# Performance work log

Measured on AMD Instinct MI355X. Metric: run time of the kernel, lower is better.

## Reference

```python
import jax, jax.numpy as jnp
import numpy as np

B, N, D_IN, D_HID, N_ITER = 32, 512, 256, 128, 10


def setup_inputs() -> dict:
    key = jax.random.key(0)
    ks = jax.random.split(key, 8)
    s = 1.0 / np.sqrt(D_IN)  # torch Linear default init range
    return {
        "Xh": jax.random.normal(ks[0], (B, N, D_IN), jnp.float32),
        "Xm": jax.random.normal(ks[1], (B, N, D_IN), jnp.float32),
        # position 0 is the root; tokens 1..len are valid
        "lengths": jax.random.randint(ks[2], (B,), N // 2, N),
        "Wh": jax.random.uniform(ks[3], (D_HID, D_IN), jnp.float32, -s, s),
        "bh": jax.random.uniform(ks[4], (D_HID,), jnp.float32, -s, s),
        "Wm": jax.random.uniform(ks[5], (D_HID, D_IN), jnp.float32, -s, s),
        "bm": jax.random.uniform(ks[6], (D_HID,), jnp.float32, -s, s),
        "V": 0.01 * jax.random.normal(ks[7], (D_HID, D_HID), jnp.float32),
    }


def _logZ(scores, lengths):
    """Matrix-tree log-partition for single-root nonprojective trees.

    scores: [B,N,N] arc scores, scores[b,h,m] = head h -> modifier m, index 0 = root.
    lengths: [B] number of real tokens (valid modifiers at 1..len).
    """
    Bn, Nn, _ = scores.shape
    idx = jnp.arange(Nn)
    tok = (idx[None, :] >= 1) & (idx[None, :] <= lengths[:, None])   # [B,N] valid modifiers
    head = idx[None, :] <= lengths[:, None]                          # [B,N] valid heads (incl. root)
    pair = head[:, :, None] & tok[:, None, :] & (idx[:, None] != idx[None, :])
    # stability shift: every tree has exactly `len` edges, so logZ shifts by len*c
    c = jax.lax.stop_gradient(
        jnp.max(jnp.where(pair, scores, -jnp.inf), axis=(1, 2)))
    A = jnp.where(pair, jnp.exp(scores - c[:, None, None]), 0.0)     # [B,N,N]
    r = A[:, 0, 1:]                                                  # root -> token weights [B,N-1]
    At = A[:, 1:, 1:]                                                # token -> token weights
    ar = jnp.arange(Nn - 1)
    # Laplacian L = diag(colsum) - At (diag of At is zero by pair mask)
    Lap = (-At).at[:, ar, ar].set(r + At.sum(axis=1))
    # Koo et al. (2007): replace first row with root weights
    Lhat = Lap.at[:, 0, :].set(r)
    # padded positions: identity rows to keep det unchanged
    Lhat = Lhat.at[:, ar, ar].add(jnp.where(tok[:, 1:], 0.0, 1.0))
    _, logabs = jnp.linalg.slogdet(Lhat)
    return logabs + lengths.astype(scores.dtype) * c


def _marginals(scores, lengths):
    """nonprojective_marginals: (logZ, entropy, mu) via grad of logZ."""
    def f(s):
        lz = _logZ(s, lengths)
        return lz.sum(), lz
    (_, logZ), Y = jax.value_and_grad(f, has_aux=True)(scores)
    entr = logZ - jnp.sum(Y * scores, axis=(1, 2))
    return logZ, entr, Y


def reference(Xh, Xm, lengths, Wh, bh, Wm, bm, V):
    # dropout=0 -> H_mask/M_mask are ones
    H0 = Xh @ Wh.T + bh          # h_mlp(Xh), invariant across iterations
    M0 = Xm @ Wm.T + bm          # m_mlp(Xm)
    H = jax.nn.relu(H0)
    M = jax.nn.relu(M0)
    scores = jnp.einsum("bhu,uv,bmv->bhm", H, V, M)
    logZ, entr, Y = _marginals(scores, lengths)
    for _ in range(1, N_ITER):
        Hn = jax.nn.relu(H0 + Y @ M @ V.T)                       # _update_H
        Mn = jax.nn.relu(M0 + jnp.swapaxes(Y, -2, -1) @ H @ V)   # _update_M
        scores = jnp.einsum("bhu,uv,bmv->bhm", Hn, V, Mn)
        logZ, entr, Y = _marginals(scores, lengths)
        H, M = Hn, Mn
    return scores, logZ, Y, entr
```

## Files before the change

### kernel.cpp

```cpp
#include <hip/hip_runtime.h>
#include <math.h>

constexpr int BB = 32;
constexpr int NN_ = 512;
constexpr int DIN = 256;
constexpr int DH = 128;
constexpr int NITER = 10;
constexpr long HSTR = (long)NN_ * DH;
constexpr long SSTR = (long)NN_ * NN_;
constexpr long LSTR = 512L * 512L;

__device__ __forceinline__ unsigned f2mono(float f) {
    unsigned u = __float_as_uint(f);
    return (u & 0x80000000u) ? ~u : (u | 0x80000000u);
}
__device__ __forceinline__ float mono2f(unsigned u) {
    return __uint_as_float((u & 0x80000000u) ? (u & 0x7fffffffu) : ~u);
}

__device__ __forceinline__ float invert128(float r[8][8], int tid,
        float (*RowP)[8][132], float (*ColPT)[8][132], float (*Rnew)[8][132])
{
    int tx = tid & 15, ty = tid >> 4;
    int lane = tid & 63, w = tid >> 6;
    int li = lane >> 3, lj = lane & 7;
    const bool act = (tid < 256);
    float lacc = 0.f;
    __syncthreads();
    for (int s8 = 0; s8 < 16; ++s8) {
        int p = s8 & 1;
        if (act && ty == s8) {
            #pragma unroll
            for (int i = 0; i < 8; ++i)
                #pragma unroll
                for (int j = 0; j < 8; ++j)
                    RowP[p][i][tx * 8 + j] = r[i][j];
        }
        if (act && tx == s8) {
            float sub = (ty == s8) ? 1.f : 0.f;
            #pragma unroll
            for (int i = 0; i < 8; ++i)
                #pragma unroll
                for (int j = 0; j < 8; ++j)
                    ColPT[p][j][ty * 8 + i] = r[i][j] - ((i == j) ? sub : 0.f);
        }
        __syncthreads();
        float d = RowP[p][li][s8 * 8 + lj];
        float prod = 1.f;
        #pragma unroll
        for (int s = 0; s < 8; ++s) {
            float pv = __shfl(d, s * 9);
            prod *= pv;
            float pinv = 1.0f / pv;
            float rv = __shfl(d, s * 8 + lj);
            float cv = __shfl(d, li * 8 + s);
            float nd;
            if (li == s && lj == s)  nd = pinv;
            else if (li == s)        nd = rv * pinv;
            else if (lj == s)        nd = -cv * pinv;
            else                     nd = d - cv * pinv * rv;
            d = nd;
        }
        lacc += logf(fabsf(prod));
        if (act) {
            int sr = li;
            int jq = w * 32 + lj * 4;
            float dsr[8];
            #pragma unroll
            for (int t = 0; t < 8; ++t) dsr[t] = __shfl(d, (lane & 56) + t);
            float a0 = 0.f, a1 = 0.f, a2 = 0.f, a3 = 0.f;
            #pragma unroll
            for (int t = 0; t < 8; ++t) {
                float4 rp = *(const float4*)&RowP[p][t][jq];
                a0 += dsr[t] * rp.x; a1 += dsr[t] * rp.y;
                a2 += dsr[t] * rp.z; a3 += dsr[t] * rp.w;
            }
            if ((jq >> 3) == s8) {
                if ((jq & 7) == 0) {
                    a0 = dsr[0] + ((sr == 0) ? 1.f : 0.f);
                    a1 = dsr[1] + ((sr == 1) ? 1.f : 0.f);
                    a2 = dsr[2] + ((sr == 2) ? 1.f : 0.f);
                    a3 = dsr[3] + ((sr == 3) ? 1.f : 0.f);
                } else {
                    a0 = dsr[4] + ((sr == 4) ? 1.f : 0.f);
                    a1 = dsr[5] + ((sr == 5) ? 1.f : 0.f);
                    a2 = dsr[6] + ((sr == 6) ? 1.f : 0.f);
                    a3 = dsr[7] + ((sr == 7) ? 1.f : 0.f);
                }
            }
            *(float4*)&Rnew[p][sr][jq] = make_float4(a0, a1, a2, a3);
        }
        __syncthreads();
        if (act) {
            #pragma unroll
            for (int t = 0; t < 8; ++t) {
                float cp[8], rn[8];
                *(float4*)&cp[0] = *(const float4*)&ColPT[p][t][ty * 8];
                *(float4*)&cp[4] = *(const float4*)&ColPT[p][t][ty * 8 + 4];
                *(float4*)&rn[0] = *(const float4*)&Rnew[p][t][tx * 8];
                *(float4*)&rn[4] = *(const float4*)&Rnew[p][t][tx * 8 + 4];
                #pragma unroll
                for (int i = 0; i < 8; ++i)
                    #pragma unroll
                    for (int j = 0; j < 8; ++j)
                        r[i][j] -= cp[i] * rn[j];
            }
        }
    }
    return lacc;
}

template<int AMODE, int BMODE, int EPI>
__global__ __launch_bounds__(256) void gemm64(
    const float* __restrict__ A, const float* __restrict__ Bm,
    float* __restrict__ C, const float* __restrict__ Dp, float* __restrict__ C2,
    int Mdim, int Ndim, int Kdim,
    long sA, long sB, long sC, long sD)
{
    constexpr int BK = 16;
    __shared__ float As[BK][64 + 4];
    __shared__ float Bs[BK][64 + 4];
    int b = blockIdx.z;
    const float* Ab = A + (long)b * sA;
    const float* Bb = Bm + (long)b * sB;
    int m0 = blockIdx.x * 64, n0 = blockIdx.y * 64;
    int tid = threadIdx.x;
    int tx = tid & 15, ty = tid >> 4;
    float acc[4][4] = {};

    int arow, acol, brow, bcol;
    if (AMODE == 0) { arow = tid >> 2; acol = (tid & 3) * 4; }
    else            { arow = tid >> 4; acol = (tid & 15) * 4; }
    if (BMODE == 0) { brow = tid >> 4; bcol = (tid & 15) * 4; }
    else            { brow = tid >> 2; bcol = (tid & 3) * 4; }

    float4 av, bv;
    if (AMODE == 0) av = *(const float4*)(Ab + (long)(m0 + arow) * Kdim + acol);
    else            av = *(const float4*)(Ab + (long)(0 + arow) * Mdim + m0 + acol);
    if (BMODE == 0) bv = *(const float4*)(Bb + (long)(0 + brow) * Ndim + n0 + bcol);
    else            bv = *(const float4*)(Bb + (long)(n0 + brow) * Kdim + bcol);

    for (int k0 = 0; k0 < Kdim; k0 += BK) {
        __syncthreads();
        if (AMODE == 0) {
            As[acol + 0][arow] = av.x; As[acol + 1][arow] = av.y;
            As[acol + 2][arow] = av.z; As[acol + 3][arow] = av.w;
        } else {
            *(float4*)&As[arow][acol] = av;
        }
        if (BMODE == 0) {
            *(float4*)&Bs[brow][bcol] = bv;
        } else {
            Bs[bcol + 0][brow] = bv.x; Bs[bcol + 1][brow] = bv.y;
            Bs[bcol + 2][brow] = bv.z; Bs[bcol + 3][brow] = bv.w;
        }
        float4 av2, bv2;
        if (k0 + BK < Kdim) {
            int k1 = k0 + BK;
            if (AMODE == 0) av2 = *(const float4*)(Ab + (long)(m0 + arow) * Kdim + k1 + acol);
            else            av2 = *(const float4*)(Ab + (long)(k1 + arow) * Mdim + m0 + acol);
            if (BMODE == 0) bv2 = *(const float4*)(Bb + (long)(k1 + brow) * Ndim + n0 + bcol);
            else            bv2 = *(const float4*)(Bb + (long)(n0 + brow) * Kdim + k1 + bcol);
        }
        __syncthreads();
        #pragma unroll
        for (int k = 0; k < BK; ++k) {
            float4 a4 = *(const float4*)&As[k][ty * 4];
            float4 b4 = *(const float4*)&Bs[k][tx * 4];
            float avv[4] = {a4.x, a4.y, a4.z, a4.w};
            float bvv[4] = {b4.x, b4.y, b4.z, b4.w};
            #pragma unroll
            for (int i = 0; i < 4; ++i)
                #pragma unroll
                for (int j = 0; j < 4; ++j)
                    acc[i][j] += avv[i] * bvv[j];
        }
        av = av2; bv = bv2;
    }

    int r0 = m0 + ty * 4, c0 = n0 + tx * 4;
    if (EPI == 0) {
        float* Cb = C + (long)b * sC;
        #pragma unroll
        for (int i = 0; i < 4; ++i)
            *(float4*)(Cb + (long)(r0 + i) * Ndim + c0) =
                make_float4(acc[i][0], acc[i][1], acc[i][2], acc[i][3]);
    } else if (EPI == 1) {
        float4 bias = *(const float4*)(Dp + c0);
        float bb4[4] = {bias.x, bias.y, bias.z, bias.w};
        #pragma unroll
        for (int i = 0; i < 4; ++i) {
            float pre[4];
            #pragma unroll
            for (int j = 0; j < 4; ++j) pre[j] = acc[i][j] + bb4[j];
            *(float4*)(C2 + (long)(r0 + i) * Ndim + c0) =
                make_float4(pre[0], pre[1], pre[2], pre[3]);
            *(float4*)(C + (long)(r0 + i) * Ndim + c0) =
                make_float4(fmaxf(pre[0], 0.f), fmaxf(pre[1], 0.f),
                            fmaxf(pre[2], 0.f), fmaxf(pre[3], 0.f));
        }
    } else {
        const float* Db = Dp + (long)b * sD;
        float* Cb = C + (long)b * sC;
        #pragma unroll
        for (int i = 0; i < 4; ++i) {
            float4 d = *(const float4*)(Db + (long)(r0 + i) * Ndim + c0);
            float pre[4] = {acc[i][0] + d.x, acc[i][1] + d.y,
                            acc[i][2] + d.z, acc[i][3] + d.w};
            *(float4*)(Cb + (long)(r0 + i) * Ndim + c0) =
                make_float4(fmaxf(pre[0], 0.f), fmaxf(pre[1], 0.f),
                            fmaxf(pre[2], 0.f), fmaxf(pre[3], 0.f));
        }
    }
}

template<int AMODE>
__global__ __launch_bounds__(256) void gemm32(
    const float* __restrict__ A, const float* __restrict__ Bm,
    float* __restrict__ C, const float* __restrict__ Dp,
    int Mdim, int Ndim, int Kdim,
    long sA, long sB, long sC, long sD)
{
    constexpr int BK = 16;
    __shared__ float As[BK][36];
    __shared__ float Bs[BK][68];
    int b = blockIdx.z;
    const float* Ab = A + (long)b * sA;
    const float* Bb = Bm + (long)b * sB;
    int m0 = blockIdx.x * 32, n0 = blockIdx.y * 64;
    int tid = threadIdx.x;
    int tx = tid & 15, ty = tid >> 4;
    float acc[2][4] = {};

    int arow, acol;
    if (AMODE == 0) { arow = tid >> 2; acol = (tid & 3) * 4; }
    else            { arow = tid >> 3; acol = (tid & 7) * 4; }
    bool aload = (tid < 128);
    int brow = tid >> 4, bcol = (tid & 15) * 4;

    float4 av, bv;
    if (aload) {
        if (AMODE == 0) av = *(const float4*)(Ab + (long)(m0 + arow) * Kdim + acol);
        else            av = *(const float4*)(Ab + (long)arow * Mdim + m0 + acol);
    }
    bv = *(const float4*)(Bb + (long)brow * Ndim + n0 + bcol);

    for (int k0 = 0; k0 < Kdim; k0 += BK) {
        __syncthreads();
        if (aload) {
            if (AMODE == 0) {
                As[acol + 0][arow] = av.x; As[acol + 1][arow] = av.y;
                As[acol + 2][arow] = av.z; As[acol + 3][arow] = av.w;
            } else {
                *(float4*)&As[arow][acol] = av;
            }
        }
        *(float4*)&Bs[brow][bcol] = bv;
        float4 av2, bv2;
        if (k0 + BK < Kdim) {
            int k1 = k0 + BK;
            if (aload) {
                if (AMODE == 0) av2 = *(const float4*)(Ab + (long)(m0 + arow) * Kdim + k1 + acol);
                else            av2 = *(const float4*)(Ab + (long)(k1 + arow) * Mdim + m0 + acol);
            }
            bv2 = *(const float4*)(Bb + (long)(k1 + brow) * Ndim + n0 + bcol);
        }
        __syncthreads();
        #pragma unroll
        for (int k = 0; k < BK; ++k) {
            float a0 = As[k][ty * 2], a1 = As[k][ty * 2 + 1];
            float4 b4 = *(const float4*)&Bs[k][tx * 4];
            float bb[4] = {b4.x, b4.y, b4.z, b4.w};
            #pragma unroll
            for (int j = 0; j < 4; ++j) {
                acc[0][j] += a0 * bb[j];
                acc[1][j] += a1 * bb[j];
            }
        }
        av = av2; bv = bv2;
    }

    int r0 = m0 + ty * 2, c0 = n0 + tx * 4;
    const float* Db = Dp + (long)b * sD;
    float* Cb = C + (long)b * sC;
    #pragma unroll
    for (int i = 0; i < 2; ++i) {
        float4 d = *(const float4*)(Db + (long)(r0 + i) * Ndim + c0);
        float pre[4] = {acc[i][0] + d.x, acc[i][1] + d.y,
                        acc[i][2] + d.z, acc[i][3] + d.w};
        *(float4*)(Cb + (long)(r0 + i) * Ndim + c0) =
            make_float4(fmaxf(pre[0], 0.f), fmaxf(pre[1], 0.f),
                        fmaxf(pre[2], 0.f), fmaxf(pre[3], 0.f));
    }
}

__global__ __launch_bounds__(256) void score_gemm(
    const float* __restrict__ A, const float* __restrict__ Bm,
    float* __restrict__ C, const int* __restrict__ len,
    unsigned* __restrict__ cu)
{
    int b = blockIdx.z;
    const float* Ab = A + (long)b * HSTR;
    const float* Bb = Bm + (long)b * HSTR;
    int m0 = blockIdx.x * 128, n0 = blockIdx.y * 128;
    int tid = threadIdx.x, tx = tid & 15, ty = tid >> 4;
    __shared__ float As[8][132];
    __shared__ float Bs[8][132];
    float acc[8][8] = {};
    int row = tid >> 1, kq = (tid & 1) << 2;
    float4 av = *(const float4*)(Ab + (long)(m0 + row) * DH + kq);
    float4 bv = *(const float4*)(Bb + (long)(n0 + row) * DH + kq);
    for (int kc = 0; kc < DH; kc += 8) {
        __syncthreads();
        As[kq + 0][row] = av.x; As[kq + 1][row] = av.y;
        As[kq + 2][row] = av.z; As[kq + 3][row] = av.w;
        Bs[kq + 0][row] = bv.x; Bs[kq + 1][row] = bv.y;
        Bs[kq + 2][row] = bv.z; Bs[kq + 3][row] = bv.w;
        float4 av2, bv2;
        if (kc + 8 < DH) {
            av2 = *(const float4*)(Ab + (long)(m0 + row) * DH + kc + 8 + kq);
            bv2 = *(const float4*)(Bb + (long)(n0 + row) * DH + kc + 8 + kq);
        }
        __syncthreads();
        #pragma unroll
        for (int k = 0; k < 8; ++k) {
            float a[8], bb[8];
            *(float4*)&a[0] = *(float4*)&As[k][ty * 8];
            *(float4*)&a[4] = *(float4*)&As[k][ty * 8 + 4];
            *(float4*)&bb[0] = *(float4*)&Bs[k][tx * 8];
            *(float4*)&bb[4] = *(float4*)&Bs[k][tx * 8 + 4];
            #pragma unroll
            for (int i = 0; i < 8; ++i)
                #pragma unroll
                for (int j = 0; j < 8; ++j) acc[i][j] += a[i] * bb[j];
        }
        av = av2; bv = bv2;
    }
    int L = len[b];
    float vmax = -3.0e38f;
    float* Cb = C + (long)b * SSTR;
    #pragma unroll
    for (int i = 0; i < 8; ++i) {
        int h = m0 + ty * 8 + i;
        bool hok = (h <= L);
        *(float4*)(Cb + (long)h * NN_ + n0 + tx * 8) =
            make_float4(acc[i][0], acc[i][1], acc[i][2], acc[i][3]);
        *(float4*)(Cb + (long)h * NN_ + n0 + tx * 8 + 4) =
            make_float4(acc[i][4], acc[i][5], acc[i][6], acc[i][7]);
        #pragma unroll
        for (int j = 0; j < 8; ++j) {
            int m = n0 + tx * 8 + j;
            if (hok && m >= 1 && m <= L && m != h) vmax = fmaxf(vmax, acc[i][j]);
        }
    }
    __syncthreads();
    float* red = &As[0][0];
    red[tid] = vmax; __syncthreads();
    for (int off = 128; off; off >>= 1) {
        if (tid < off) red[tid] = fmaxf(red[tid], red[tid + off]);
        __syncthreads();
    }
    if (tid == 0) atomicMax(&cu[b], f2mono(red[0]));
}

__global__ void zero_scal(float* scal) {
    if (threadIdx.x < 96) scal[threadIdx.x] = 0.f;
}

__global__ __launch_bounds__(256) void colsum_k(const float* __restrict__ sc,
                                                const int* __restrict__ len,
                                                const unsigned* __restrict__ cu,
                                                float* __restrict__ colsum)
{
    int b = blockIdx.x, yb = blockIdx.y;
    int tid = threadIdx.x, lane = tid & 63, w = tid >> 6;
    int L = len[b];
    float c = mono2f(cu[b]);
    int m = yb * 64 + lane;
    const float* S = sc + (long)b * SSTR;
    float s = 0.f;
    bool mv = (m >= 1 && m <= L);
    if (mv) {
        for (int h = 1 + w; h < NN_; h += 4) {
            if (h <= L && h != m) s += expf(S[(long)h * NN_ + m] - c);
        }
    }
    __shared__ float part[4][64];
    part[w][lane] = s; __syncthreads();
    if (tid < 64)
        colsum[(long)b * NN_ + yb * 64 + tid] =
            part[0][tid] + part[1][tid] + part[2][tid] + part[3][tid];
}

__global__ __launch_bounds__(256) void build_diag0(const float* __restrict__ sc,
                                                   const int* __restrict__ len,
                                                   const unsigned* __restrict__ cu,
                                                   const float* __restrict__ colsum,
                                                   float* __restrict__ Lm,
                                                   float* __restrict__ logdet)
{
    __shared__ float sm[6][8][132];
    int b = blockIdx.x;
    int tid = threadIdx.x;
    int L = len[b];
    float c = mono2f(cu[b]);
    const float* S = sc + (long)b * SSTR;
    const float* cs = colsum + (long)b * NN_;
    int tx = tid & 15, ty = tid >> 4;
    float r[8][8];
    #pragma unroll
    for (int i = 0; i < 8; ++i) {
        int gi = ty * 8 + i;
        #pragma unroll
        for (int j = 0; j < 8; ++j) {
            int gj = tx * 8 + j;
            int tm = gj + 1;
            bool mv = (tm <= L);
            float v;
            if (gi == 0) {
                v = mv ? expf(S[tm] - c) : 0.f;
            } else if (gi == gj) {
                float rv = mv ? expf(S[tm] - c) : 0.f;
                v = rv + cs[tm] + (mv ? 0.f : 1.f);
            } else {
                int h = gi + 1;
                v = (h <= L && mv) ? -expf(S[(long)h * NN_ + tm] - c) : 0.f;
            }
            r[i][j] = v;
        }
    }
    float lacc = invert128(r, tid,
                           (float(*)[8][132])&sm[0],
                           (float(*)[8][132])&sm[2],
                           (float(*)[8][132])&sm[4]);
    float* Ab = Lm + (long)b * LSTR;
    #pragma unroll
    for (int i = 0; i < 8; ++i) {
        *(float4*)(Ab + (long)(ty * 8 + i) * 512 + tx * 8) =
            make_float4(r[i][0], r[i][1], r[i][2], r[i][3]);
        *(float4*)(Ab + (long)(ty * 8 + i) * 512 + tx * 8 + 4) =
            make_float4(r[i][4], r[i][5], r[i][6], r[i][7]);
    }
    if (tid == 0) atomicAdd(&logdet[b], lacc);
}

__global__ __launch_bounds__(256) void build_rows(const float* __restrict__ sc,
                                                  const int* __restrict__ len,
                                                  const unsigned* __restrict__ cu,
                                                  const float* __restrict__ colsum,
                                                  float* __restrict__ Lm,
                                                  float* __restrict__ Fb0)
{
    int b = blockIdx.x;
    int tid = threadIdx.x;
    int L = len[b];
    float c = mono2f(cu[b]);
    const float* S = sc + (long)b * SSTR;
    const float* cs = colsum + (long)b * NN_;

    int i0 = blockIdx.y * 8;
    #pragma unroll
    for (int r = 0; r < 8; ++r) {
        int i = i0 + r;
        float* Lrow = Lm + (long)b * LSTR + (long)i * 512;
        float* Frow = Fb0 + (long)b * HSTR + (long)i * 128;
        #pragma unroll
        for (int q = 0; q < 2; ++q) {
            int j = tid + q * 256;
            float v;
            if (i == 511 || j == 511) {
                v = (i == j) ? 1.f : 0.f;
            } else {
                int tm = j + 1;
                bool mv = (tm <= L);
                if (i == 0) {
                    v = mv ? expf(S[tm] - c) : 0.f;
                } else if (i == j) {
                    float rv = mv ? expf(S[tm] - c) : 0.f;
                    v = rv + cs[tm] + ((tm > L) ? 1.f : 0.f);
                } else {
                    int h = i + 1;
                    v = (h <= L && mv) ? -expf(S[(long)h * NN_ + tm] - c) : 0.f;
                }
            }
            if (!(i < 128 && j < 128)) Lrow[j] = v;
            if (q == 0 && j < 128 && i >= 128) Frow[j] = v;
        }
    }
}

__global__ __launch_bounds__(256) void gj_panel(float* __restrict__ Lm,
                                                float* __restrict__ Fnext, int kb)
{
    constexpr int BK = 16;
    __shared__ float Ds[BK][132];
    __shared__ float As2[BK][36];
    int b = blockIdx.x;
    int j = blockIdx.y >> 2;
    int cq = blockIdx.y & 3;
    int jt = j + (j >= kb);
    int c0 = cq * 32;
    int tid = threadIdx.x;
    int tx = tid & 7, ty = tid >> 3;
    float* base = Lm + (long)b * LSTR;
    const float* D = base + (long)(kb * 128) * 512 + kb * 128;
    float* Aj = base + (long)(kb * 128) * 512 + jt * 128;
    int drow = tid >> 1, dk8 = (tid & 1) * 8;
    int akr = tid >> 3, acq4 = (tid & 7) * 4;
    bool aload = (akr < BK);
    float acc[4][4] = {};
    float4 dva = *(const float4*)(D + (long)drow * 512 + dk8);
    float4 dvb = *(const float4*)(D + (long)drow * 512 + dk8 + 4);
    float4 av;
    if (aload) av = *(const float4*)(Aj + (long)akr * 512 + c0 + acq4);
    for (int kc = 0; kc < 128; kc += BK) {
        __syncthreads();
        Ds[dk8 + 0][drow] = dva.x; Ds[dk8 + 1][drow] = dva.y;
        Ds[dk8 + 2][drow] = dva.z; Ds[dk8 + 3][drow] = dva.w;
        Ds[dk8 + 4][drow] = dvb.x; Ds[dk8 + 5][drow] = dvb.y;
        Ds[dk8 + 6][drow] = dvb.z; Ds[dk8 + 7][drow] = dvb.w;
        if (aload) *(float4*)&As2[akr][acq4] = av;
        float4 dva2, dvb2, av2;
        if (kc + BK < 128) {
            dva2 = *(const float4*)(D + (long)drow * 512 + kc + BK + dk8);
            dvb2 = *(const float4*)(D + (long)drow * 512 + kc + BK + dk8 + 4);
            if (aload) av2 = *(const float4*)(Aj + (long)(kc + BK + akr) * 512 + c0 + acq4);
        }
        __syncthreads();
        #pragma unroll
        for (int k = 0; k < BK; ++k) {
            float4 a4 = *(const float4*)&Ds[k][ty * 4];
            float4 b4 = *(const float4*)&As2[k][tx * 4];
            float a[4] = {a4.x, a4.y, a4.z, a4.w};
            float bb[4] = {b4.x, b4.y, b4.z, b4.w};
            #pragma unroll
            for (int i = 0; i < 4; ++i)
                #pragma unroll
                for (int jj = 0; jj < 4; ++jj)
                    acc[i][jj] += a[i] * bb[jj];
        }
        dva = dva2; dvb = dvb2; av = av2;
    }
    bool dual = (jt == kb + 1);
    float* Fn = Fnext + (long)b * HSTR + (long)(kb * 128) * 128;
    #pragma unroll
    for (int i = 0; i < 4; ++i) {
        float4 o = make_float4(acc[i][0], acc[i][1], acc[i][2], acc[i][3]);
        *(float4*)(Aj + (long)(ty * 4 + i) * 512 + c0 + tx * 4) = o;
        if (dual) *(float4*)(Fn + (long)(ty * 4 + i) * 128 + c0 + tx * 4) = o;
    }
}

__global__ __launch_bounds__(256) void gj_update64(
    float* __restrict__ Lm, const float* __restrict__ Fbuf,
    float* __restrict__ Fnext, float* __restrict__ logdet, int kb)
{
    constexpr int BK = 16;
    __shared__ float sm[6 * 8 * 132];
    int b = blockIdx.x;
    int tid = threadIdx.x;
    float* base = Lm + (long)b * LSTR;

    if (blockIdx.z == 0) {
        if (blockIdx.y != 0 || kb >= 3) return;
        int dt = kb + 1;
        const float* F = Fbuf + (long)b * HSTR + (long)(dt * 128) * 128;
        const float* R = base + (long)(kb * 128) * 512 + dt * 128;
        float* Cb = base + (long)(dt * 128) * 512 + dt * 128;
        float (*Fs)[132] = (float (*)[132])sm;
        float (*Rs)[132] = (float (*)[132])(sm + 16 * 132);
        int tx = tid & 15, ty = tid >> 4;
        int frow = tid >> 1, fkq = (tid & 1) << 3;
        int rkr = tid >> 4, rcq = (tid & 15) << 3;
        float acc[8][8] = {};
        float4 fva = *(const float4*)(F + (long)frow * 128 + fkq);
        float4 fvb = *(const float4*)(F + (long)frow * 128 + fkq + 4);
        float4 rva = *(const float4*)(R + (long)rkr * 512 + rcq);
        float4 rvb = *(const float4*)(R + (long)rkr * 512 + rcq + 4);
        for (int kc = 0; kc < 128; kc += BK) {
            __syncthreads();
            Fs[fkq + 0][frow] = fva.x; Fs[fkq + 1][frow] = fva.y;
            Fs[fkq + 2][frow] = fva.z; Fs[fkq + 3][frow] = fva.w;
            Fs[fkq + 4][frow] = fvb.x; Fs[fkq + 5][frow] = fvb.y;
            Fs[fkq + 6][frow] = fvb.z; Fs[fkq + 7][frow] = fvb.w;
            *(float4*)&Rs[rkr][rcq] = rva;
            *(float4*)&Rs[rkr][rcq + 4] = rvb;
            float4 fva2, fvb2, rva2, rvb2;
            if (kc + BK < 128) {
                fva2 = *(const float4*)(F + (long)frow * 128 + kc + BK + fkq);
                fvb2 = *(const float4*)(F + (long)frow * 128 + kc + BK + fkq + 4);
                rva2 = *(const float4*)(R + (long)(kc + BK + rkr) * 512 + rcq);
                rvb2 = *(const float4*)(R + (long)(kc + BK + rkr) * 512 + rcq + 4);
            }
            __syncthreads();
            #pragma unroll
            for (int k = 0; k < BK; ++k) {
                float a[8], bb[8];
                *(float4*)&a[0] = *(const float4*)&Fs[k][ty * 8];
                *(float4*)&a[4] = *(const float4*)&Fs[k][ty * 8 + 4];
                *(float4*)&bb[0] = *(const float4*)&Rs[k][tx * 8];
                *(float4*)&bb[4] = *(const float4*)&Rs[k][tx * 8 + 4];
                #pragma unroll
                for (int i = 0; i < 8; ++i)
                    #pragma unroll
                    for (int j = 0; j < 8; ++j)
                        acc[i][j] += a[i] * bb[j];
            }
            fva = fva2; fvb = fvb2; rva = rva2; rvb = rvb2;
        }
        #pragma unroll
        for (int i = 0; i < 8; ++i) {
            float4 o0 = *(const float4*)(Cb + (long)(ty * 8 + i) * 512 + tx * 8);
            float4 o1 = *(const float4*)(Cb + (long)(ty * 8 + i) * 512 + tx * 8 + 4);
            acc[i][0] = o0.x - acc[i][0]; acc[i][1] = o0.y - acc[i][1];
            acc[i][2] = o0.z - acc[i][2]; acc[i][3] = o0.w - acc[i][3];
            acc[i][4] = o1.x - acc[i][4]; acc[i][5] = o1.y - acc[i][5];
            acc[i][6] = o1.z - acc[i][6]; acc[i][7] = o1.w - acc[i][7];
        }
        float lacc = invert128(acc, tid,
                               (float (*)[8][132])sm,
                               (float (*)[8][132])(sm + 2 * 8 * 132),
                               (float (*)[8][132])(sm + 4 * 8 * 132));
        #pragma unroll
        for (int i = 0; i < 8; ++i) {
            *(float4*)(Cb + (long)(ty * 8 + i) * 512 + tx * 8) =
                make_float4(acc[i][0], acc[i][1], acc[i][2], acc[i][3]);
            *(float4*)(Cb + (long)(ty * 8 + i) * 512 + tx * 8 + 4) =
                make_float4(acc[i][4], acc[i][5], acc[i][6], acc[i][7]);
        }
        if (tid == 0) atomicAdd(&logdet[b], lacc);
        return;
    }

    float (*Fs)[68] = (float (*)[68])sm;
    float (*Rs)[68] = (float (*)[68])(sm + BK * 68);
    int it = blockIdx.y;
    int ib = it + (it >= kb);
    int sub = blockIdx.z - 1;
    int jt = sub >> 2;
    int quad = sub & 3;
    if (kb < 3 && ib == kb + 1 && jt == kb + 1) return;
    int r0 = (quad >> 1) * 64, c0 = (quad & 1) * 64;
    int tx = tid & 15, ty = tid >> 4;
    const float* F = Fbuf + (long)b * HSTR + (long)(ib * 128 + r0) * 128;
    const float* R = base + (long)(kb * 128) * 512 + jt * 128 + c0;
    float* Cb = base + (long)(ib * 128 + r0) * 512 + jt * 128 + c0;
    int frow = tid >> 2, fkq = (tid & 3) << 2;
    int rkr = tid >> 4, rcq = (tid & 15) << 2;
    float acc[4][4] = {};
    float4 fv = *(const float4*)(F + (long)frow * 128 + fkq);
    float4 rv = *(const float4*)(R + (long)rkr * 512 + rcq);
    for (int kc = 0; kc < 128; kc += BK) {
        __syncthreads();
        Fs[fkq + 0][frow] = fv.x; Fs[fkq + 1][frow] = fv.y;
        Fs[fkq + 2][frow] = fv.z; Fs[fkq + 3][frow] = fv.w;
        *(float4*)&Rs[rkr][rcq] = rv;
        float4 fv2, rv2;
        if (kc + BK < 128) {
            fv2 = *(const float4*)(F + (long)frow * 128 + kc + BK + fkq);
            rv2 = *(const float4*)(R + (long)(kc + BK + rkr) * 512 + rcq);
        }
        __syncthreads();
        #pragma unroll
        for (int k = 0; k < BK; ++k) {
            float4 a4 = *(const float4*)&Fs[k][ty * 4];
            float4 b4 = *(const float4*)&Rs[k][tx * 4];
            float a[4] = {a4.x, a4.y, a4.z, a4.w};
            float bb[4] = {b4.x, b4.y, b4.z, b4.w};
            #pragma unroll
            for (int i = 0; i < 4; ++i)
                #pragma unroll
                for (int j = 0; j < 4; ++j)
                    acc[i][j] += a[i] * bb[j];
        }
        fv = fv2; rv = rv2;
    }
    bool dual = (jt == kb + 1);
    float* Fn = Fnext + (long)b * HSTR + (long)(ib * 128 + r0) * 128 + c0;
    if (jt == kb) {
        #pragma unroll
        for (int i = 0; i < 4; ++i)
            *(float4*)(Cb + (long)(ty * 4 + i) * 512 + tx * 4) =
                make_float4(-acc[i][0], -acc[i][1], -acc[i][2], -acc[i][3]);
    } else {
        #pragma unroll
        for (int i = 0; i < 4; ++i) {
            float4 o = *(const float4*)(Cb + (long)(ty * 4 + i) * 512 + tx * 4);
            o = make_float4(o.x - acc[i][0], o.y - acc[i][1],
                            o.z - acc[i][2], o.w - acc[i][3]);
            *(float4*)(Cb + (long)(ty * 4 + i) * 512 + tx * 4) = o;
            if (dual) *(float4*)(Fn + (long)(ty * 4 + i) * 128 + tx * 4) = o;
        }
    }
}

__global__ __launch_bounds__(256) void y_k(const float* __restrict__ sc,
                                           const float* __restrict__ Binv,
                                           const int* __restrict__ len,
                                           const unsigned* __restrict__ cu,
                                           float* __restrict__ Y,
                                           float* __restrict__ Ssum)
{
    int b = blockIdx.x;
    int ht = blockIdx.y >> 3, mt = blockIdx.y & 7;
    int h0 = ht * 64, m0 = mt * 64;
    int tid = threadIdx.x;
    int L = len[b];
    float c = mono2f(cu[b]);
    const float* S = sc + (long)b * SSTR;
    const float* Bi = Binv + (long)b * LSTR;
    float* Yb = Y + (long)b * SSTR;
    __shared__ float Bs[64][65];
    __shared__ float Ds[64], C0s[64];
    {
        int hh = tid & 63, m4 = tid >> 6;
        int col = h0 + hh - 1;
        for (int mm = m4; mm < 64; mm += 4) {
            int row = m0 + mm - 1;
            Bs[mm][hh] = (row >= 0 && col >= 0) ? Bi[(long)row * 512 + col] : 0.f;
        }
    }
    if (tid < 64) {
        int row = m0 + tid - 1;
        Ds[tid] = (row >= 0) ? Bi[(long)row * 512 + row] : 0.f;
    } else if (tid < 128) {
        int mm = tid - 64, row = m0 + mm - 1;
        C0s[mm] = (row >= 0) ? Bi[(long)row * 512] : 0.f;
    }
    __syncthreads();
    int mm = tid & 63, hq = tid >> 6;
    int m = m0 + mm;
    float lsum = 0.f;
    bool mvalid = (m >= 1 && m <= L);
    float dterm = (m >= 2) ? Ds[mm] : 0.f;
    #pragma unroll
    for (int hi = 0; hi < 16; ++hi) {
        int hh = hq * 16 + hi;
        int h = h0 + hh;
        float s = S[(long)h * NN_ + m];
        float y = 0.f;
        if (mvalid && h <= L && h != m) {
            float a = expf(s - c);
            float g;
            if (h == 0) g = C0s[mm] + dterm;
            else g = dterm - ((h >= 2) ? Bs[mm][hh] : 0.f);
            y = a * g;
        }
        Yb[(long)h * NN_ + m] = y;
        lsum += y * s;
    }
    __shared__ float red[256];
    red[tid] = lsum; __syncthreads();
    for (int off = 128; off; off >>= 1) {
        if (tid < off) red[tid] += red[tid + off];
        __syncthreads();
    }
    if (tid == 0) atomicAdd(&Ssum[b], red[0]);
}

__global__ void fin_k(const int* __restrict__ len, unsigned* __restrict__ cu,
                      float* __restrict__ logdet, float* __restrict__ Ssum,
                      float* __restrict__ outLogZ, float* __restrict__ outEntr)
{
    int b = threadIdx.x;
    if (b < 32) {
        float c = mono2f(cu[b]);
        float lz = logdet[b] + (float)len[b] * c;
        outLogZ[b] = lz;
        outEntr[b] = lz - Ssum[b];
        cu[b] = 0u;
        logdet[b] = 0.f;
        Ssum[b] = 0.f;
    }
}

extern "C" void kernel_launch(void* const* d_in, const int* in_sizes, int n_in,
                              void* d_out, int out_size, void* d_ws, size_t ws_size,
                              hipStream_t stream)
{
    const float* Xh = (const float*)d_in[0];
    const float* Xm = (const float*)d_in[1];
    const int*   len = (const int*)d_in[2];
    const float* Wh = (const float*)d_in[3];
    const float* bh = (const float*)d_in[4];
    const float* Wm = (const float*)d_in[5];
    const float* bm = (const float*)d_in[6];
    const float* V  = (const float*)d_in[7];

    float* ws = (float*)d_ws;
    constexpr long U = 2097152;
    float* H0 = ws;
    float* M0 = ws + U;
    float* Ha = ws + 2 * U;
    float* Ma = ws + 3 * U;
    float* Hb = ws + 4 * U;
    float* Mb = ws + 5 * U;
    float* T1 = ws + 6 * U;
    float* Yt = ws + 7 * U;
    float* Lm = ws + 8 * U;
    float* cs = ws + 12 * U;
    float* scal = ws + 12 * U + 16384;
    unsigned* cu = (unsigned*)scal;
    float* logdet = scal + 32;
    float* Ssum = scal + 64;

    float* Sout = (float*)d_out;
    float* outLogZ = (float*)d_out + 8388608;
    float* Yout = (float*)d_out + 8388640;
    float* outEntr = (float*)d_out + 8388640 + 8388608;

    zero_scal<<<1, 96, 0, stream>>>(scal);

    gemm64<0,1,1><<<dim3(256, 2, 1), 256, 0, stream>>>(
        Xh, Wh, Ha, bh, H0, 16384, DH, DIN, 0, 0, 0, 0);
    gemm64<0,1,1><<<dim3(256, 2, 1), 256, 0, stream>>>(
        Xm, Wm, Ma, bm, M0, 16384, DH, DIN, 0, 0, 0, 0);

    float* Hc = Ha; float* Mc = Ma; float* Hn = Hb; float* Mn = Mb;
    for (int t = 0; t < NITER; ++t) {
        if (t > 0) {
            gemm64<0,1,0><<<dim3(8,2,BB),256,0,stream>>>(
                Mc, V, Yt, nullptr, nullptr, 512, DH, DH, HSTR, 0, HSTR, 0);
            gemm32<0><<<dim3(16,2,BB),256,0,stream>>>(
                Yout, Yt, Hn, H0, 512, DH, 512, SSTR, HSTR, HSTR, HSTR);
            gemm32<1><<<dim3(16,2,BB),256,0,stream>>>(
                Yout, T1, Mn, M0, 512, DH, 512, SSTR, HSTR, HSTR, HSTR);
            { float* tmp = Hc; Hc = Hn; Hn = tmp; }
            { float* tmp = Mc; Mc = Mn; Mn = tmp; }
        }
        gemm64<0,0,0><<<dim3(8,2,BB),256,0,stream>>>(
            Hc, V, T1, nullptr, nullptr, 512, DH, DH, HSTR, 0, HSTR, 0);
        score_gemm<<<dim3(4,4,BB),256,0,stream>>>(T1, Mc, Sout, len, cu);

        colsum_k<<<dim3(BB,8),256,0,stream>>>(Sout, len, cu, cs);
        build_diag0<<<dim3(BB),256,0,stream>>>(Sout, len, cu, cs, Lm, logdet);
        build_rows<<<dim3(BB,64),256,0,stream>>>(Sout, len, cu, cs, Lm, Yt);

        float* Fbufs[2] = {Yt, Hn};
        for (int kb = 0; kb < 4; ++kb) {
            float* Fcur  = Fbufs[kb & 1];
            float* Fnext = Fbufs[(kb + 1) & 1];
            gj_panel<<<dim3(BB,12),256,0,stream>>>(Lm, Fnext, kb);
            gj_update64<<<dim3(BB,3,17),256,0,stream>>>(Lm, Fcur, Fnext, logdet, kb);
        }
        y_k<<<dim3(BB,64),256,0,stream>>>(Sout, Lm, len, cu, Yout, Ssum);
        fin_k<<<1,32,0,stream>>>(len, cu, logdet, Ssum, outLogZ, outEntr);
    }
}
```

Before: 5.538 ms.

## Move next diagonal-block inversion into panel kernel to shorten critical path

The lookahead step (updating and inverting the next 128x128 diagonal block) moves from the update kernel into an extra block of the panel kernel. That block computes D·A for the next column panel into scratch, then applies the Schur update and inversion. The update kernel can then start without a long-running inversion block trailing behind it. The cost is recomputing the panel product redundantly in one block, and it adds a scratch buffer (reusing Mn) plus a threadfence. The dual-write panel tile now goes only to Fnext, and the update kernel reads it from there.

```diff
diff --git a/kernel.cpp b/kernel.cpp
--- a/kernel.cpp
+++ b/kernel.cpp
@@ -489,20 +489,146 @@
     }
 }
 
-__global__ __launch_bounds__(256) void gj_panel(float* __restrict__ Lm,
-                                                float* __restrict__ Fnext, int kb)
+__global__ __launch_bounds__(256) void gj_panel(
+    float* __restrict__ Lm, const float* __restrict__ Fcur,
+    float* __restrict__ Fnext, float* __restrict__ Rscr,
+    float* __restrict__ logdet, int kb)
 {
     constexpr int BK = 16;
-    __shared__ float Ds[BK][132];
-    __shared__ float As2[BK][36];
+    __shared__ float sm[6 * 8 * 132];
     int b = blockIdx.x;
+    int tid = threadIdx.x;
+    float* base = Lm + (long)b * LSTR;
+
+    if (blockIdx.y == 12) {
+        if (kb >= 3) return;
+        int dt = kb + 1;
+        int tx = tid & 15, ty = tid >> 4;
+        float (*Xs)[132] = (float (*)[132])sm;
+        float (*Ys)[132] = (float (*)[132])(sm + 16 * 132);
+        int xr = tid >> 1, xk = (tid & 1) << 3;
+        int yk = tid >> 4, yc = (tid & 15) << 3;
+        float* Rb = Rscr + (long)b * 16384;
+        {
+            const float* Dv = base + (long)(kb * 128) * 512 + kb * 128;
+            const float* Am = base + (long)(kb * 128) * 512 + dt * 128;
+            float acc[8][8] = {};
+            float4 xa = *(const float4*)(Dv + (long)xr * 512 + xk);
+            float4 xb = *(const float4*)(Dv + (long)xr * 512 + xk + 4);
+            float4 ya = *(const float4*)(Am + (long)yk * 512 + yc);
+            float4 yb = *(const float4*)(Am + (long)yk * 512 + yc + 4);
+            for (int kc = 0; kc < 128; kc += BK) {
+                __syncthreads();
+                Xs[xk + 0][xr] = xa.x; Xs[xk + 1][xr] = xa.y;
+                Xs[xk + 2][xr] = xa.z; Xs[xk + 3][xr] = xa.w;
+                Xs[xk + 4][xr] = xb.x; Xs[xk + 5][xr] = xb.y;
+                Xs[xk + 6][xr] = xb.z; Xs[xk + 7][xr] = xb.w;
+                *(float4*)&Ys[yk][yc] = ya;
+                *(float4*)&Ys[yk][yc + 4] = yb;
+                float4 xa2, xb2, ya2, yb2;
+                if (kc + BK < 128) {
+                    xa2 = *(const float4*)(Dv + (long)xr * 512 + kc + BK + xk);
+                    xb2 = *(const float4*)(Dv + (long)xr * 512 + kc + BK + xk + 4);
+                    ya2 = *(const float4*)(Am + (long)(kc + BK + yk) * 512 + yc);
+                    yb2 = *(const float4*)(Am + (long)(kc + BK + yk) * 512 + yc + 4);
+                }
+                __syncthreads();
+                #pragma unroll
+                for (int k = 0; k < BK; ++k) {
+                    float a[8], bb[8];
+                    *(float4*)&a[0] = *(const float4*)&Xs[k][ty * 8];
+                    *(float4*)&a[4] = *(const float4*)&Xs[k][ty * 8 + 4];
+                    *(float4*)&bb[0] = *(const float4*)&Ys[k][tx * 8];
+                    *(float4*)&bb[4] = *(const float4*)&Ys[k][tx * 8 + 4];
+                    #pragma unroll
+                    for (int i = 0; i < 8; ++i)
+                        #pragma unroll
+                        for (int j = 0; j < 8; ++j)
+                            acc[i][j] += a[i] * bb[j];
+                }
+                xa = xa2; xb = xb2; ya = ya2; yb = yb2;
+            }
+            #pragma unroll
+            for (int i = 0; i < 8; ++i) {
+                *(float4*)(Rb + (long)(ty * 8 + i) * 128 + tx * 8) =
+                    make_float4(acc[i][0], acc[i][1], acc[i][2], acc[i][3]);
+                *(float4*)(Rb + (long)(ty * 8 + i) * 128 + tx * 8 + 4) =
+                    make_float4(acc[i][4], acc[i][5], acc[i][6], acc[i][7]);
+            }
+        }
+        __threadfence();
+        __syncthreads();
+        {
+            const float* F = Fcur + (long)b * HSTR + (long)(dt * 128) * 128;
+            float* Cb = base + (long)(dt * 128) * 512 + dt * 128;
+            float acc[8][8] = {};
+            float4 xa = *(const float4*)(F + (long)xr * 128 + xk);
+            float4 xb = *(const float4*)(F + (long)xr * 128 + xk + 4);
+            float4 ya = *(const float4*)(Rb + (long)yk * 128 + yc);
+            float4 yb = *(const float4*)(Rb + (long)yk * 128 + yc + 4);
+            for (int kc = 0; kc < 128; kc += BK) {
+                __syncthreads();
+                Xs[xk + 0][xr] = xa.x; Xs[xk + 1][xr] = xa.y;
+                Xs[xk + 2][xr] = xa.z; Xs[xk + 3][xr] = xa.w;
+                Xs[xk + 4][xr] = xb.x; Xs[xk + 5][xr] = xb.y;
+                Xs[xk + 6][xr] = xb.z; Xs[xk + 7][xr] = xb.w;
+                *(float4*)&Ys[yk][yc] = ya;
+                *(float4*)&Ys[yk][yc + 4] = yb;
+                float4 xa2, xb2, ya2, yb2;
+                if (kc + BK < 128) {
+                    xa2 = *(const float4*)(F + (long)xr * 128 + kc + BK + xk);
+                    xb2 = *(const float4*)(F + (long)xr * 128 + kc + BK + xk + 4);
+                    ya2 = *(const float4*)(Rb + (long)(kc + BK + yk) * 128 + yc);
+                    yb2 = *(const float4*)(Rb + (long)(kc + BK + yk) * 128 + yc + 4);
+                }
+                __syncthreads();
+                #pragma unroll
+                for (int k = 0; k < BK; ++k) {
+                    float a[8], bb[8];
+                    *(float4*)&a[0] = *(const float4*)&Xs[k][ty * 8];
+                    *(float4*)&a[4] = *(const float4*)&Xs[k][ty * 8 + 4];
+                    *(float4*)&bb[0] = *(const float4*)&Ys[k][tx * 8];
+                    *(float4*)&bb[4] = *(const float4*)&Ys[k][tx * 8 + 4];
+                    #pragma unroll
+                    for (int i = 0; i < 8; ++i)
+                        #pragma unroll
+                        for (int j = 0; j < 8; ++j)
+                            acc[i][j] += a[i] * bb[j];
+                }
+                xa = xa2; xb = xb2; ya = ya2; yb = yb2;
+            }
+            #pragma unroll
+            for (int i = 0; i < 8; ++i) {
+                float4 o0 = *(const float4*)(Cb + (long)(ty * 8 + i) * 512 + tx * 8);
+                float4 o1 = *(const float4*)(Cb + (long)(ty * 8 + i) * 512 + tx * 8 + 4);
+                acc[i][0] = o0.x - acc[i][0]; acc[i][1] = o0.y - acc[i][1];
+                acc[i][2] = o0.z - acc[i][2]; acc[i][3] = o0.w - acc[i][3];
+                acc[i][4] = o1.x - acc[i][4]; acc[i][5] = o1.y - acc[i][5];
+                acc[i][6] = o1.z - acc[i][6]; acc[i][7] = o1.w - acc[i][7];
+            }
+            float lacc = invert128(acc, tid,
+                                   (float (*)[8][132])sm,
+                                   (float (*)[8][132])(sm + 2 * 8 * 132),
+                                   (float (*)[8][132])(sm + 4 * 8 * 132));
+            #pragma unroll
+            for (int i = 0; i < 8; ++i) {
+                *(float4*)(Cb + (long)(ty * 8 + i) * 512 + tx * 8) =
+                    make_float4(acc[i][0], acc[i][1], acc[i][2], acc[i][3]);
+                *(float4*)(Cb + (long)(ty * 8 + i) * 512 + tx * 8 + 4) =
+                    make_float4(acc[i][4], acc[i][5], acc[i][6], acc[i][7]);
+            }
+            if (tid == 0) atomicAdd(&logdet[b], lacc);
+        }
+        return;
+    }
+
+    float (*Ds)[132] = (float (*)[132])sm;
+    float (*As2)[36] = (float (*)[36])(sm + 16 * 132);
     int j = blockIdx.y >> 2;
     int cq = blockIdx.y & 3;
     int jt = j + (j >= kb);
     int c0 = cq * 32;
-    int tid = threadIdx.x;
     int tx = tid & 7, ty = tid >> 3;
-    float* base = Lm + (long)b * LSTR;
     const float* D = base + (long)(kb * 128) * 512 + kb * 128;
     float* Aj = base + (long)(kb * 128) * 512 + jt * 128;
     int drow = tid >> 1, dk8 = (tid & 1) * 8;
@@ -546,110 +672,45 @@
     #pragma unroll
     for (int i = 0; i < 4; ++i) {
         float4 o = make_float4(acc[i][0], acc[i][1], acc[i][2], acc[i][3]);
-        *(float4*)(Aj + (long)(ty * 4 + i) * 512 + c0 + tx * 4) = o;
         if (dual) *(float4*)(Fn + (long)(ty * 4 + i) * 128 + c0 + tx * 4) = o;
+        else      *(float4*)(Aj + (long)(ty * 4 + i) * 512 + c0 + tx * 4) = o;
     }
 }
 
 __global__ __launch_bounds__(256) void gj_update64(
     float* __restrict__ Lm, const float* __restrict__ Fbuf,
-    float* __restrict__ Fnext, float* __restrict__ logdet, int kb)
+    float* __restrict__ Fnext, int kb)
 {
     constexpr int BK = 16;
-    __shared__ float sm[6 * 8 * 132];
+    __shared__ float Fs[BK][68];
+    __shared__ float Rs[BK][68];
     int b = blockIdx.x;
-    int tid = threadIdx.x;
-    float* base = Lm + (long)b * LSTR;
-
-    if (blockIdx.z == 0) {
-        if (blockIdx.y != 0 || kb >= 3) return;
-        int dt = kb + 1;
-        const float* F = Fbuf + (long)b * HSTR + (long)(dt * 128) * 128;
-        const float* R = base + (long)(kb * 128) * 512 + dt * 128;
-        float* Cb = base + (long)(dt * 128) * 512 + dt * 128;
-        float (*Fs)[132] = (float (*)[132])sm;
-        float (*Rs)[132] = (float (*)[132])(sm + 16 * 132);
-        int tx = tid & 15, ty = tid >> 4;
-        int frow = tid >> 1, fkq = (tid & 1) << 3;
-        int rkr = tid >> 4, rcq = (tid & 15) << 3;
-        float acc[8][8] = {};
-        float4 fva = *(const float4*)(F + (long)frow * 128 + fkq);
-        float4 fvb = *(const float4*)(F + (long)frow * 128 + fkq + 4);
-        float4 rva = *(const float4*)(R + (long)rkr * 512 + rcq);
-        float4 rvb = *(const float4*)(R + (long)rkr * 512 + rcq + 4);
-        for (int kc = 0; kc < 128; kc += BK) {
-            __syncthreads();
-            Fs[fkq + 0][frow] = fva.x; Fs[fkq + 1][frow] = fva.y;
-            Fs[fkq + 2][frow] = fva.z; Fs[fkq + 3][frow] = fva.w;
-            Fs[fkq + 4][frow] = fvb.x; Fs[fkq + 5][frow] = fvb.y;
-            Fs[fkq + 6][frow] = fvb.z; Fs[fkq + 7][frow] = fvb.w;
-            *(float4*)&Rs[rkr][rcq] = rva;
-            *(float4*)&Rs[rkr][rcq + 4] = rvb;
-            float4 fva2, fvb2, rva2, rvb2;
-            if (kc + BK < 128) {
-                fva2 = *(const float4*)(F + (long)frow * 128 + kc + BK + fkq);
-                fvb2 = *(const float4*)(F + (long)frow * 128 + kc + BK + fkq + 4);
-                rva2 = *(const float4*)(R + (long)(kc + BK + rkr) * 512 + rcq);
-                rvb2 = *(const float4*)(R + (long)(kc + BK + rkr) * 512 + rcq + 4);
-            }
-            __syncthreads();
-            #pragma unroll
-            for (int k = 0; k < BK; ++k) {
-                float a[8], bb[8];
-                *(float4*)&a[0] = *(const float4*)&Fs[k][ty * 8];
-                *(float4*)&a[4] = *(const float4*)&Fs[k][ty * 8 + 4];
-                *(float4*)&bb[0] = *(const float4*)&Rs[k][tx * 8];
-                *(float4*)&bb[4] = *(const float4*)&Rs[k][tx * 8 + 4];
-                #pragma unroll
-                for (int i = 0; i < 8; ++i)
-                    #pragma unroll
-                    for (int j = 0; j < 8; ++j)
-                        acc[i][j] += a[i] * bb[j];
-            }
-            fva = fva2; fvb = fvb2; rva = rva2; rvb = rvb2;
-        }
-        #pragma unroll
-        for (int i = 0; i < 8; ++i) {
-            float4 o0 = *(const float4*)(Cb + (long)(ty * 8 + i) * 512 + tx * 8);
-            float4 o1 = *(const float4*)(Cb + (long)(ty * 8 + i) * 512 + tx * 8 + 4);
-            acc[i][0] = o0.x - acc[i][0]; acc[i][1] = o0.y - acc[i][1];
-            acc[i][2] = o0.z - acc[i][2]; acc[i][3] = o0.w - acc[i][3];
-            acc[i][4] = o1.x - acc[i][4]; acc[i][5] = o1.y - acc[i][5];
-            acc[i][6] = o1.z - acc[i][6]; acc[i][7] = o1.w - acc[i][7];
-        }
-        float lacc = invert128(acc, tid,
-                               (float (*)[8][132])sm,
-                               (float (*)[8][132])(sm + 2 * 8 * 132),
-                               (float (*)[8][132])(sm + 4 * 8 * 132));
-        #pragma unroll
-        for (int i = 0; i < 8; ++i) {
-            *(float4*)(Cb + (long)(ty * 8 + i) * 512 + tx * 8) =
-                make_float4(acc[i][0], acc[i][1], acc[i][2], acc[i][3]);
-            *(float4*)(Cb + (long)(ty * 8 + i) * 512 + tx * 8 + 4) =
-                make_float4(acc[i][4], acc[i][5], acc[i][6], acc[i][7]);
-        }
-        if (tid == 0) atomicAdd(&logdet[b], lacc);
-        return;
-    }
-
-    float (*Fs)[68] = (float (*)[68])sm;
-    float (*Rs)[68] = (float (*)[68])(sm + BK * 68);
     int it = blockIdx.y;
     int ib = it + (it >= kb);
-    int sub = blockIdx.z - 1;
+    int sub = blockIdx.z;
     int jt = sub >> 2;
     int quad = sub & 3;
     if (kb < 3 && ib == kb + 1 && jt == kb + 1) return;
     int r0 = (quad >> 1) * 64, c0 = (quad & 1) * 64;
+    int tid = threadIdx.x;
     int tx = tid & 15, ty = tid >> 4;
+    float* base = Lm + (long)b * LSTR;
     const float* F = Fbuf + (long)b * HSTR + (long)(ib * 128 + r0) * 128;
-    const float* R = base + (long)(kb * 128) * 512 + jt * 128 + c0;
+    const float* R;
+    long ldR;
+    if (jt == kb + 1) {
+        R = Fnext + (long)b * HSTR + (long)(kb * 128) * 128 + c0;
+        ldR = 128;
+    } else {
+        R = base + (long)(kb * 128) * 512 + (long)jt * 128 + c0;
+        ldR = 512;
+    }
     float* Cb = base + (long)(ib * 128 + r0) * 512 + jt * 128 + c0;
     int frow = tid >> 2, fkq = (tid & 3) << 2;
     int rkr = tid >> 4, rcq = (tid & 15) << 2;
     float acc[4][4] = {};
     float4 fv = *(const float4*)(F + (long)frow * 128 + fkq);
-    float4 rv = *(const float4*)(R + (long)rkr * 512 + rcq);
+    float4 rv = *(const float4*)(R + (long)rkr * ldR + rcq);
     for (int kc = 0; kc < 128; kc += BK) {
         __syncthreads();
         Fs[fkq + 0][frow] = fv.x; Fs[fkq + 1][frow] = fv.y;
@@ -658,7 +719,7 @@
         float4 fv2, rv2;
         if (kc + BK < 128) {
             fv2 = *(const float4*)(F + (long)frow * 128 + kc + BK + fkq);
-            rv2 = *(const float4*)(R + (long)(kc + BK + rkr) * 512 + rcq);
+            rv2 = *(const float4*)(R + (long)(kc + BK + rkr) * ldR + rcq);
         }
         __syncthreads();
         #pragma unroll
@@ -840,8 +901,8 @@
         for (int kb = 0; kb < 4; ++kb) {
             float* Fcur  = Fbufs[kb & 1];
             float* Fnext = Fbufs[(kb + 1) & 1];
-            gj_panel<<<dim3(BB,12),256,0,stream>>>(Lm, Fnext, kb);
-            gj_update64<<<dim3(BB,3,17),256,0,stream>>>(Lm, Fcur, Fnext, logdet, kb);
+            gj_panel<<<dim3(BB,13),256,0,stream>>>(Lm, Fcur, Fnext, Mn, logdet, kb);
+            gj_update64<<<dim3(BB,3,16),256,0,stream>>>(Lm, Fcur, Fnext, kb);
         }
         y_k<<<dim3(BB,64),256,0,stream>>>(Sout, Lm, len, cu, Yout, Ssum);
         fin_k<<<1,32,0,stream>>>(len, cu, logdet, Ssum, outLogZ, outEntr);
```

Measured after the change: 6.686 ms. 20.7% more time.
